# Performance work log

Measured on AMD Instinct MI355X. Metric: run time of the kernel, lower is better.

The kernel has to match this reference:

```python
import math
import jax, jax.numpy as jnp
import numpy as np

DIM = 3
N_LEVELS = 16
N_FEATS = 2
LOG2_HASHMAP = 19
BASE_RES = 16
FINEST_RES = 512

_b = math.exp((math.log(FINEST_RES) - math.log(BASE_RES)) / (N_LEVELS - 1))
LEVEL_RES = []
LEVEL_SIZE = []
for _l in range(N_LEVELS):
    _res = math.floor(BASE_RES * _b ** _l)
    _sz = min(_res ** DIM, 2 ** LOG2_HASHMAP)
    _sz = 2 ** math.ceil(math.log2(_sz))
    LEVEL_RES.append(_res)
    LEVEL_SIZE.append(_sz)
MAX_SIZE = max(LEVEL_SIZE)  # 2**19

PRIMES_U32 = jnp.asarray([1, 2654435761, 805459861], dtype=jnp.uint32)
# bin_mask[n, d] == True  <->  bit d of neighbor index n is 0 (take floor corner on dim d)
_neigs = np.arange(1 << DIM, dtype=np.int64).reshape(-1, 1)
_dims = np.arange(DIM, dtype=np.int64).reshape(1, -1)
BIN_MASK = jnp.asarray((_neigs & (1 << _dims)) == 0)  # [8, 3] bool


def _level_encode(x, table, resolution, hashmap_size):
    """x: [N, 3] in [0,1); table: [hashmap_size, F] -> [N, F]."""
    xs = x * resolution                       # [N, 3]
    xi = jnp.floor(xs)                        # grid cell corner (float)
    xf = xs - jax.lax.stop_gradient(xi)       # fractional part, grad flows like torch's detach
    xi_u = xi.astype(jnp.uint32)[:, None, :]  # [N, 1, 3]
    xf = xf[:, None, :]                       # [N, 1, 3]
    inds = jnp.where(BIN_MASK, xi_u, xi_u + jnp.uint32(1))   # [N, 8, 3]
    ws = jnp.where(BIN_MASK, 1.0 - xf, xf)                    # [N, 8, 3]
    w = jnp.prod(ws, axis=-1, keepdims=True)                  # [N, 8, 1]
    # tiny-cuda-nn hash: xor of per-dim (coord * prime), then mod table size (power of 2)
    u = inds * PRIMES_U32                                     # uint32 wraparound == & 0xFFFFFFFF
    h = u[..., 0] ^ u[..., 1] ^ u[..., 2]                     # [N, 8]
    hid = (h & jnp.uint32(hashmap_size - 1)).astype(jnp.int32)
    neig = table[hid]                                         # [N, 8, F] gather
    return jnp.sum(neig * w, axis=-2)                         # [N, F]


def setup_inputs() -> dict:
    key = jax.random.key(0)
    kx, kt = jax.random.split(key)
    x = jax.random.uniform(kx, (2097152, DIM), dtype=jnp.float32)
    tables = jax.random.uniform(kt, (N_LEVELS, MAX_SIZE, N_FEATS), dtype=jnp.float32,
                                minval=-1e-4, maxval=1e-4)
    return {"x": x, "tables": tables}


def reference(x, tables):
    outs = [
        _level_encode(x, tables[l, :LEVEL_SIZE[l]], float(LEVEL_RES[l]), LEVEL_SIZE[l])
        for l in range(N_LEVELS)
    ]
    return jnp.concatenate(outs, axis=-1)  # [N, n_levels * n_features]
```

## Files before the change

kernel.cpp:

```cpp
#include <hip/hip_runtime.h>
#include <math.h>

#define N_LEVELS 16
#define MAX_SIZE (1u << 19)

struct Params {
    float res[N_LEVELS];
    unsigned int mask[N_LEVELS];
};

__global__ __launch_bounds__(256) void hashgrid_level_kernel(
    const float* __restrict__ x,
    const float* __restrict__ tables,
    float2* __restrict__ ws,
    Params p, int N)
{
    int l = blockIdx.y;
    int n = blockIdx.x * 256 + threadIdx.x;
    if (n >= N) return;

    float res = p.res[l];
    unsigned int mask = p.mask[l];
    const float2* __restrict__ tab =
        reinterpret_cast<const float2*>(tables) + (size_t)l * MAX_SIZE;

    float px = x[n * 3 + 0];
    float py = x[n * 3 + 1];
    float pz = x[n * 3 + 2];

    float xs = px * res, ys = py * res, zs = pz * res;
    float fxi = floorf(xs), fyi = floorf(ys), fzi = floorf(zs);
    float wx1 = xs - fxi, wy1 = ys - fyi, wz1 = zs - fzi;
    float wx0 = 1.0f - wx1, wy0 = 1.0f - wy1, wz0 = 1.0f - wz1;

    unsigned int ix = (unsigned int)fxi;
    unsigned int iy = (unsigned int)fyi;
    unsigned int iz = (unsigned int)fzi;

    const unsigned int P2 = 2654435761u, P3 = 805459861u;
    unsigned int hx0 = ix;       unsigned int hx1 = ix + 1u;
    unsigned int hy0 = iy * P2;  unsigned int hy1 = hy0 + P2;
    unsigned int hz0 = iz * P3;  unsigned int hz1 = hz0 + P3;

    unsigned int hidx[8];
    float w[8];
#pragma unroll
    for (int c = 0; c < 8; ++c) {
        unsigned int hh = ((c & 1) ? hx1 : hx0)
                        ^ ((c & 2) ? hy1 : hy0)
                        ^ ((c & 4) ? hz1 : hz0);
        hidx[c] = hh & mask;
        w[c] = (((c & 1) ? wx1 : wx0) * ((c & 2) ? wy1 : wy0)) * ((c & 4) ? wz1 : wz0);
    }

    float2 v[8];
#pragma unroll
    for (int c = 0; c < 8; ++c) v[c] = tab[hidx[c]];

    float accx = 0.0f, accy = 0.0f;
#pragma unroll
    for (int c = 0; c < 8; ++c) {
        accx += v[c].x * w[c];
        accy += v[c].y * w[c];
    }

    ws[(size_t)l * N + n] = make_float2(accx, accy);
}

__global__ __launch_bounds__(256) void transpose_kernel(
    const float2* __restrict__ ws,
    float2* __restrict__ out,
    int N)
{
    __shared__ float2 lds[N_LEVELS][257];
    int tid = threadIdx.x;
    int n0 = blockIdx.x * 256;
    int n = n0 + tid;

#pragma unroll
    for (int l = 0; l < N_LEVELS; ++l) {
        if (n < N) lds[l][tid] = ws[(size_t)l * N + n];
    }
    __syncthreads();

#pragma unroll
    for (int i = 0; i < 16; ++i) {
        int pn = i * 16 + (tid >> 4);
        int j  = tid & 15;
        int np = n0 + pn;
        if (np < N) out[(size_t)np * 16 + j] = lds[j][pn];
    }
}

__global__ __launch_bounds__(256) void hashgrid_kernel(
    const float* __restrict__ x,
    const float* __restrict__ tables,
    float2* __restrict__ out,
    Params p, int total)
{
    int t = blockIdx.x * 256 + threadIdx.x;
    if (t >= total) return;
    int l = t & 15;
    int n = t >> 4;

    float res = p.res[l];
    unsigned int mask = p.mask[l];
    const float2* __restrict__ tab =
        reinterpret_cast<const float2*>(tables) + (size_t)l * MAX_SIZE;

    float px = x[n * 3 + 0];
    float py = x[n * 3 + 1];
    float pz = x[n * 3 + 2];

    float xs = px * res, ys = py * res, zs = pz * res;
    float fxi = floorf(xs), fyi = floorf(ys), fzi = floorf(zs);
    float wx1 = xs - fxi, wy1 = ys - fyi, wz1 = zs - fzi;
    float wx0 = 1.0f - wx1, wy0 = 1.0f - wy1, wz0 = 1.0f - wz1;

    unsigned int ix = (unsigned int)fxi;
    unsigned int iy = (unsigned int)fyi;
    unsigned int iz = (unsigned int)fzi;

    const unsigned int P2 = 2654435761u, P3 = 805459861u;
    unsigned int hx0 = ix;       unsigned int hx1 = ix + 1u;
    unsigned int hy0 = iy * P2;  unsigned int hy1 = hy0 + P2;
    unsigned int hz0 = iz * P3;  unsigned int hz1 = hz0 + P3;

    unsigned int hidx[8];
    float w[8];
#pragma unroll
    for (int c = 0; c < 8; ++c) {
        unsigned int hh = ((c & 1) ? hx1 : hx0)
                        ^ ((c & 2) ? hy1 : hy0)
                        ^ ((c & 4) ? hz1 : hz0);
        hidx[c] = hh & mask;
        w[c] = (((c & 1) ? wx1 : wx0) * ((c & 2) ? wy1 : wy0)) * ((c & 4) ? wz1 : wz0);
    }

    float2 v[8];
#pragma unroll
    for (int c = 0; c < 8; ++c) v[c] = tab[hidx[c]];

    float accx = 0.0f, accy = 0.0f;
#pragma unroll
    for (int c = 0; c < 8; ++c) {
        accx += v[c].x * w[c];
        accy += v[c].y * w[c];
    }

    out[t] = make_float2(accx, accy);
}

extern "C" void kernel_launch(void* const* d_in, const int* in_sizes, int n_in,
                              void* d_out, int out_size, void* d_ws, size_t ws_size,
                              hipStream_t stream) {
    const float* x      = (const float*)d_in[0];
    const float* tables = (const float*)d_in[1];
    float2* out         = (float2*)d_out;

    int N = in_sizes[0] / 3;

    Params p;
    double b = exp((log(512.0) - log(16.0)) / 15.0);
    for (int l = 0; l < N_LEVELS; ++l) {
        double r = floor(16.0 * pow(b, (double)l));
        long long res = (long long)r;
        long long cube = res * res * res;
        long long sz = cube < (long long)(1u << 19) ? cube : (long long)(1u << 19);
        unsigned int pw = 1;
        while ((long long)pw < sz) pw <<= 1;
        p.res[l]  = (float)r;
        p.mask[l] = pw - 1u;
    }

    size_t ws_needed = (size_t)N * N_LEVELS * sizeof(float2);
    int bpl = (N + 255) / 256;

    if (ws_size >= ws_needed) {
        dim3 grid1(bpl, N_LEVELS, 1);
        hashgrid_level_kernel<<<grid1, 256, 0, stream>>>(
            x, tables, (float2*)d_ws, p, N);
        transpose_kernel<<<bpl, 256, 0, stream>>>(
            (const float2*)d_ws, out, N);
    } else {
        int total = N * N_LEVELS;
        int blocks = (total + 255) / 256;
        hashgrid_kernel<<<blocks, 256, 0, stream>>>(x, tables, out, p, total);
    }
}
```

Before: 1.010 ms.

## Group levels into cache-budgeted phases and use nontemporal streaming accesses

Consecutive levels are packed into phases whose combined table size fits a host-chosen byte budget (about 3.5 MB). Each thread loops over the levels of one phase, so x is loaded once per phase instead of once per level and the tables in play stay small enough to remain cached. Loads of x and stores and loads of the workspace and output are marked nontemporal so streaming data does not evict table lines. The trade-off is fewer blocks in the grid and a serial loop per thread, which lowers parallelism for the phases that hold several small levels.

New measurement: 984.3 us. 2.6% less time.

```diff
diff --git a/kernel.cpp b/kernel.cpp
--- a/kernel.cpp
+++ b/kernel.cpp
@@ -3,68 +3,77 @@
 
 #define N_LEVELS 16
 #define MAX_SIZE (1u << 19)
+
+typedef float f2v __attribute__((ext_vector_type(2)));
 
 struct Params {
     float res[N_LEVELS];
     unsigned int mask[N_LEVELS];
+    int lstart[N_LEVELS + 1];
 };
 
-__global__ __launch_bounds__(256) void hashgrid_level_kernel(
+__global__ __launch_bounds__(256) void hashgrid_phase_kernel(
     const float* __restrict__ x,
     const float* __restrict__ tables,
     float2* __restrict__ ws,
     Params p, int N)
 {
-    int l = blockIdx.y;
+    int ph = blockIdx.y;
     int n = blockIdx.x * 256 + threadIdx.x;
     if (n >= N) return;
 
-    float res = p.res[l];
-    unsigned int mask = p.mask[l];
-    const float2* __restrict__ tab =
-        reinterpret_cast<const float2*>(tables) + (size_t)l * MAX_SIZE;
-
-    float px = x[n * 3 + 0];
-    float py = x[n * 3 + 1];
-    float pz = x[n * 3 + 2];
-
-    float xs = px * res, ys = py * res, zs = pz * res;
-    float fxi = floorf(xs), fyi = floorf(ys), fzi = floorf(zs);
-    float wx1 = xs - fxi, wy1 = ys - fyi, wz1 = zs - fzi;
-    float wx0 = 1.0f - wx1, wy0 = 1.0f - wy1, wz0 = 1.0f - wz1;
-
-    unsigned int ix = (unsigned int)fxi;
-    unsigned int iy = (unsigned int)fyi;
-    unsigned int iz = (unsigned int)fzi;
+    float px = __builtin_nontemporal_load(x + (size_t)n * 3 + 0);
+    float py = __builtin_nontemporal_load(x + (size_t)n * 3 + 1);
+    float pz = __builtin_nontemporal_load(x + (size_t)n * 3 + 2);
 
     const unsigned int P2 = 2654435761u, P3 = 805459861u;
-    unsigned int hx0 = ix;       unsigned int hx1 = ix + 1u;
-    unsigned int hy0 = iy * P2;  unsigned int hy1 = hy0 + P2;
-    unsigned int hz0 = iz * P3;  unsigned int hz1 = hz0 + P3;
-
-    unsigned int hidx[8];
-    float w[8];
-#pragma unroll
-    for (int c = 0; c < 8; ++c) {
-        unsigned int hh = ((c & 1) ? hx1 : hx0)
-                        ^ ((c & 2) ? hy1 : hy0)
-                        ^ ((c & 4) ? hz1 : hz0);
-        hidx[c] = hh & mask;
-        w[c] = (((c & 1) ? wx1 : wx0) * ((c & 2) ? wy1 : wy0)) * ((c & 4) ? wz1 : wz0);
-    }
-
-    float2 v[8];
-#pragma unroll
-    for (int c = 0; c < 8; ++c) v[c] = tab[hidx[c]];
-
-    float accx = 0.0f, accy = 0.0f;
-#pragma unroll
-    for (int c = 0; c < 8; ++c) {
-        accx += v[c].x * w[c];
-        accy += v[c].y * w[c];
-    }
-
-    ws[(size_t)l * N + n] = make_float2(accx, accy);
+
+    int l0 = p.lstart[ph], l1 = p.lstart[ph + 1];
+    for (int l = l0; l < l1; ++l) {
+        float res = p.res[l];
+        unsigned int mask = p.mask[l];
+        const float2* __restrict__ tab =
+            reinterpret_cast<const float2*>(tables) + (size_t)l * MAX_SIZE;
+
+        float xs = px * res, ys = py * res, zs = pz * res;
+        float fxi = floorf(xs), fyi = floorf(ys), fzi = floorf(zs);
+        float wx1 = xs - fxi, wy1 = ys - fyi, wz1 = zs - fzi;
+        float wx0 = 1.0f - wx1, wy0 = 1.0f - wy1, wz0 = 1.0f - wz1;
+
+        unsigned int ix = (unsigned int)fxi;
+        unsigned int iy = (unsigned int)fyi;
+        unsigned int iz = (unsigned int)fzi;
+
+        unsigned int hx0 = ix;       unsigned int hx1 = ix + 1u;
+        unsigned int hy0 = iy * P2;  unsigned int hy1 = hy0 + P2;
+        unsigned int hz0 = iz * P3;  unsigned int hz1 = hz0 + P3;
+
+        unsigned int hidx[8];
+        float w[8];
+#pragma unroll
+        for (int c = 0; c < 8; ++c) {
+            unsigned int hh = ((c & 1) ? hx1 : hx0)
+                            ^ ((c & 2) ? hy1 : hy0)
+                            ^ ((c & 4) ? hz1 : hz0);
+            hidx[c] = hh & mask;
+            w[c] = (((c & 1) ? wx1 : wx0) * ((c & 2) ? wy1 : wy0)) * ((c & 4) ? wz1 : wz0);
+        }
+
+        float2 v[8];
+#pragma unroll
+        for (int c = 0; c < 8; ++c) v[c] = tab[hidx[c]];
+
+        float accx = 0.0f, accy = 0.0f;
+#pragma unroll
+        for (int c = 0; c < 8; ++c) {
+            accx += v[c].x * w[c];
+            accy += v[c].y * w[c];
+        }
+
+        f2v r; r.x = accx; r.y = accy;
+        __builtin_nontemporal_store(
+            r, reinterpret_cast<f2v*>(&ws[(size_t)l * N + n]));
+    }
 }
 
 __global__ __launch_bounds__(256) void transpose_kernel(
@@ -79,7 +88,11 @@
 
 #pragma unroll
     for (int l = 0; l < N_LEVELS; ++l) {
-        if (n < N) lds[l][tid] = ws[(size_t)l * N + n];
+        if (n < N) {
+            f2v v = __builtin_nontemporal_load(
+                reinterpret_cast<const f2v*>(&ws[(size_t)l * N + n]));
+            lds[l][tid] = make_float2(v.x, v.y);
+        }
     }
     __syncthreads();
 
@@ -88,7 +101,12 @@
         int pn = i * 16 + (tid >> 4);
         int j  = tid & 15;
         int np = n0 + pn;
-        if (np < N) out[(size_t)np * 16 + j] = lds[j][pn];
+        if (np < N) {
+            float2 s = lds[j][pn];
+            f2v v; v.x = s.x; v.y = s.y;
+            __builtin_nontemporal_store(
+                v, reinterpret_cast<f2v*>(&out[(size_t)np * 16 + j]));
+        }
     }
 }
 
@@ -173,12 +191,28 @@
         p.mask[l] = pw - 1u;
     }
 
+    const size_t BUDGET = (size_t)(7u << 19);
+    int np = 0;
+    size_t acc = 0;
+    bool open = false;
+    for (int l = 0; l < N_LEVELS; ++l) {
+        size_t tb = ((size_t)p.mask[l] + 1) * sizeof(float2);
+        if (open && acc + tb <= BUDGET) {
+            acc += tb;
+        } else {
+            p.lstart[np++] = l;
+            acc = tb;
+            open = true;
+        }
+    }
+    p.lstart[np] = N_LEVELS;
+
     size_t ws_needed = (size_t)N * N_LEVELS * sizeof(float2);
     int bpl = (N + 255) / 256;
 
     if (ws_size >= ws_needed) {
-        dim3 grid1(bpl, N_LEVELS, 1);
-        hashgrid_level_kernel<<<grid1, 256, 0, stream>>>(
+        dim3 grid1(bpl, np, 1);
+        hashgrid_phase_kernel<<<grid1, 256, 0, stream>>>(
             x, tables, (float2*)d_ws, p, N);
         transpose_kernel<<<bpl, 256, 0, stream>>>(
             (const float2*)d_ws, out, N);
```
